# Optimization experiments

Measured on AMD Instinct MI355X. Metric: run time of the kernel, lower is better.

## Reference

```python
import jax, jax.numpy as jnp
import numpy as np

B, NX, NY, F = 4, 4096, 4096, 16

def setup_inputs() -> dict:
    key = jax.random.key(0)
    k1, k2, k3, k4, k5 = jax.random.split(key, 5)
    return {
        "x": jax.random.normal(k1, (B, NX, 3), dtype=jnp.float32),
        "y": jax.random.normal(k2, (B, NY, 3), dtype=jnp.float32),
        "sample_x": jax.random.uniform(k3, (B, NX, F), dtype=jnp.float32),
        "sample_y": jax.random.uniform(k4, (B, NY, F), dtype=jnp.float32),
        "scale": jax.random.uniform(k5, (F,), dtype=jnp.float32),
    }

def reference(x, y, sample_x, sample_y, scale):
    sq_x = jnp.sum(x * x, axis=-1, keepdims=True)            # (B,NX,1)
    sq_y = jnp.sum(y * y, axis=-1, keepdims=True)            # (B,NY,1)
    dot = jnp.einsum('bnd,bmd->bnm', x, y)                   # (B,NX,NY)
    d = jnp.clip(sq_x + jnp.swapaxes(sq_y, -2, -1) - 2.0 * dot, 1e-10, 1e6)
    # fixed-scale branch
    s = jnp.clip(scale, 1e-6, 1e6)
    scale_x = jnp.clip(jnp.einsum('bnf,f->bn', sample_x, s), 1e-10, 1e6)  # (B,NX)
    scale_y = jnp.clip(jnp.einsum('bmf,f->bm', sample_y, s), 1e-10, 1e6)  # (B,NY)
    scale_xy = jnp.sqrt(jnp.clip(scale_x[:, :, None] * scale_y[:, None, :], 1e-10, 1e12))
    return 1.0 / (1.0 + d / scale_xy)
```

## Files before the change

kernel.cpp:

```cpp
#include <hip/hip_runtime.h>


constexpr int kB  = 4;
constexpr int kNX = 4096;
constexpr int kNY = 4096;
constexpr int kF  = 16;

typedef float floatx4 __attribute__((ext_vector_type(4)));

__global__ __launch_bounds__(256) void row_stats_kernel(
    const float* __restrict__ x, const float* __restrict__ y,
    const float* __restrict__ sx, const float* __restrict__ sy,
    const float* __restrict__ scale,
    float2* __restrict__ rx, float2* __restrict__ ry, int nper)
{
    int t = blockIdx.x * blockDim.x + threadIdx.x;
    if (t >= 2 * nper) return;
    const float* pts; const float* smp; float2* dst; int idx;
    if (t < nper) { pts = x; smp = sx; dst = rx; idx = t; }
    else          { pts = y; smp = sy; dst = ry; idx = t - nper; }

    const float* p = pts + (size_t)idx * 3;
    float sq = p[0] * p[0] + p[1] * p[1] + p[2] * p[2];

    const float4* s4 = (const float4*)(smp + (size_t)idx * kF);
    const float4* c4 = (const float4*)scale;
    float acc = 0.f;
#pragma unroll
    for (int k = 0; k < kF / 4; ++k) {
        float4 sv = s4[k];
        float4 cv = c4[k];
        acc += sv.x * fminf(fmaxf(cv.x, 1e-6f), 1e6f);
        acc += sv.y * fminf(fmaxf(cv.y, 1e-6f), 1e6f);
        acc += sv.z * fminf(fmaxf(cv.z, 1e-6f), 1e6f);
        acc += sv.w * fminf(fmaxf(cv.w, 1e-6f), 1e6f);
    }
    float sc = fminf(fmaxf(acc, 1e-10f), 1e6f);
    dst[idx] = make_float2(sq, __builtin_amdgcn_sqrtf(sc));
}

__device__ __forceinline__ void cauchy_tile(
    int b, int i0, int j0,
    const float sqx[4], const float scx[4],
    const float sqy[4], const float scy[4],
    const float xxx[4], const float xyy[4], const float xzz[4],
    const float yxx[4], const float yyy[4], const float yzz[4],
    float* __restrict__ out)
{
    size_t obase = ((size_t)b * kNX + i0) * (size_t)kNY + j0;
#pragma unroll
    for (int r = 0; r < 4; ++r) {
        floatx4 o;
#pragma unroll
        for (int k = 0; k < 4; ++k) {
            float dot = xxx[r] * yxx[k] + xyy[r] * yyy[k] + xzz[r] * yzz[k];
            float d = fmaf(-2.f, dot, sqx[r] + sqy[k]);
            d = fminf(fmaxf(d, 1e-10f), 1e6f);
            float s = fmaxf(scx[r] * scy[k], 1e-5f);
            o[k] = s * __builtin_amdgcn_rcpf(s + d);
        }
        __builtin_nontemporal_store(o, (floatx4*)(out + obase + (size_t)r * kNY));
    }
}

__global__ __launch_bounds__(256) void cauchy_main_kernel(
    const float* __restrict__ x, const float* __restrict__ y,
    const float2* __restrict__ rx, const float2* __restrict__ ry,
    float* __restrict__ out)
{
    const int jc = ((blockIdx.x & 3) << 8) | threadIdx.x;
    const int rowtile = blockIdx.x >> 2;
    const int b  = rowtile >> 10;
    const int i0 = (rowtile & (kNX / 4 - 1)) << 2;
    const int j0 = jc << 2;

    const float4* yv = (const float4*)(y + ((size_t)b * kNY + j0) * 3);
    float4 ya = yv[0], yb = yv[1], yc = yv[2];
    const float4* ryv = (const float4*)(ry + (size_t)b * kNY + j0);
    float4 r01 = ryv[0], r23 = ryv[1];

    const float4* xv = (const float4*)(x + ((size_t)b * kNX + i0) * 3);
    float4 xa = xv[0], xb = xv[1], xc = xv[2];
    const float4* rxv = (const float4*)(rx + (size_t)b * kNX + i0);
    float4 q01 = rxv[0], q23 = rxv[1];

    const float yxx[4] = {ya.x, ya.w, yb.z, yc.y};
    const float yyy[4] = {ya.y, yb.x, yb.w, yc.z};
    const float yzz[4] = {ya.z, yb.y, yc.x, yc.w};
    const float sqy[4] = {r01.x, r01.z, r23.x, r23.z};
    const float scy[4] = {r01.y, r01.w, r23.y, r23.w};

    const float xxx[4] = {xa.x, xa.w, xb.z, xc.y};
    const float xyy[4] = {xa.y, xb.x, xb.w, xc.z};
    const float xzz[4] = {xa.z, xb.y, xc.x, xc.w};
    const float sqx[4] = {q01.x, q01.z, q23.x, q23.z};
    const float scx[4] = {q01.y, q01.w, q23.y, q23.w};

    cauchy_tile(b, i0, j0, sqx, scx, sqy, scy,
                xxx, xyy, xzz, yxx, yyy, yzz, out);
}

__global__ __launch_bounds__(256) void cauchy_fallback_kernel(
    const float* __restrict__ x, const float* __restrict__ y,
    const float* __restrict__ sx, const float* __restrict__ sy,
    const float* __restrict__ scale, float* __restrict__ out)
{
    const int jc = ((blockIdx.x & 3) << 8) | threadIdx.x;
    const int rowtile = blockIdx.x >> 2;
    const int b  = rowtile >> 10;
    const int i0 = (rowtile & (kNX / 4 - 1)) << 2;
    const int j0 = jc << 2;

    float4 c[4];
    const float4* c4 = (const float4*)scale;
#pragma unroll
    for (int k = 0; k < 4; ++k) {
        float4 cv = c4[k];
        c[k].x = fminf(fmaxf(cv.x, 1e-6f), 1e6f);
        c[k].y = fminf(fmaxf(cv.y, 1e-6f), 1e6f);
        c[k].z = fminf(fmaxf(cv.z, 1e-6f), 1e6f);
        c[k].w = fminf(fmaxf(cv.w, 1e-6f), 1e6f);
    }

    const float4* yv = (const float4*)(y + ((size_t)b * kNY + j0) * 3);
    float4 ya = yv[0], yb = yv[1], yc = yv[2];
    const float4* xv = (const float4*)(x + ((size_t)b * kNX + i0) * 3);
    float4 xa = xv[0], xb = xv[1], xc = xv[2];

    const float yxx[4] = {ya.x, ya.w, yb.z, yc.y};
    const float yyy[4] = {ya.y, yb.x, yb.w, yc.z};
    const float yzz[4] = {ya.z, yb.y, yc.x, yc.w};
    const float xxx[4] = {xa.x, xa.w, xb.z, xc.y};
    const float xyy[4] = {xa.y, xb.x, xb.w, xc.z};
    const float xzz[4] = {xa.z, xb.y, xc.x, xc.w};

    float sqx[4], scx[4], sqy[4], scy[4];
#pragma unroll
    for (int r = 0; r < 4; ++r) {
        sqx[r] = xxx[r] * xxx[r] + xyy[r] * xyy[r] + xzz[r] * xzz[r];
        sqy[r] = yxx[r] * yxx[r] + yyy[r] * yyy[r] + yzz[r] * yzz[r];
        const float4* a4 = (const float4*)(sx + ((size_t)b * kNX + i0 + r) * kF);
        const float4* b4 = (const float4*)(sy + ((size_t)b * kNY + j0 + r) * kF);
        float accx = 0.f, accy = 0.f;
#pragma unroll
        for (int k = 0; k < 4; ++k) {
            float4 av = a4[k], bv = b4[k], cv = c[k];
            accx += av.x * cv.x + av.y * cv.y + av.z * cv.z + av.w * cv.w;
            accy += bv.x * cv.x + bv.y * cv.y + bv.z * cv.z + bv.w * cv.w;
        }
        scx[r] = __builtin_amdgcn_sqrtf(fminf(fmaxf(accx, 1e-10f), 1e6f));
        scy[r] = __builtin_amdgcn_sqrtf(fminf(fmaxf(accy, 1e-10f), 1e6f));
    }

    cauchy_tile(b, i0, j0, sqx, scx, sqy, scy,
                xxx, xyy, xzz, yxx, yyy, yzz, out);
}

extern "C" void kernel_launch(void* const* d_in, const int* in_sizes, int n_in,
                              void* d_out, int out_size, void* d_ws, size_t ws_size,
                              hipStream_t stream) {
    const float* x     = (const float*)d_in[0];
    const float* y     = (const float*)d_in[1];
    const float* sx    = (const float*)d_in[2];
    const float* sy    = (const float*)d_in[3];
    const float* scale = (const float*)d_in[4];
    float* out = (float*)d_out;

    const int nper = kB * kNX;
    const size_t need = (size_t)2 * nper * sizeof(float2);
    const int main_blocks = (kB * kNX * kNY / 16) / 256;

    if (ws_size >= need) {
        float2* rx = (float2*)d_ws;
        float2* ry = rx + nper;
        row_stats_kernel<<<(2 * nper + 255) / 256, 256, 0, stream>>>(
            x, y, sx, sy, scale, rx, ry, nper);
        cauchy_main_kernel<<<main_blocks, 256, 0, stream>>>(x, y, rx, ry, out);
    } else {
        cauchy_fallback_kernel<<<main_blocks, 256, 0, stream>>>(
            x, y, sx, sy, scale, out);
    }
}
```

Measured before the change: 271.7 us.

## Fuse row stats into single kernel with XCD-aware block remap and plain stores

Removes the separate row-statistics pre-pass and workspace, so each thread recomputes squared norms and scale sums for its 4 x-rows and 4 y-columns from the raw sample arrays. Block indices are remapped so that consecutive logical tiles land on the same XCD, which is meant to improve L2 reuse of the x/y/sample inputs. The output stores change from nontemporal to ordinary vector stores. The cost is redundant per-thread dot products over 16 features and extra input reads, in exchange for dropping one launch and the round trip through workspace.

```diff
diff --git a/kernel.cpp b/kernel.cpp
--- a/kernel.cpp
+++ b/kernel.cpp
@@ -5,108 +5,19 @@
 constexpr int kNX = 4096;
 constexpr int kNY = 4096;
 constexpr int kF  = 16;
+constexpr int kNumXCD = 8;
 
-typedef float floatx4 __attribute__((ext_vector_type(4)));
-
-__global__ __launch_bounds__(256) void row_stats_kernel(
-    const float* __restrict__ x, const float* __restrict__ y,
-    const float* __restrict__ sx, const float* __restrict__ sy,
-    const float* __restrict__ scale,
-    float2* __restrict__ rx, float2* __restrict__ ry, int nper)
-{
-    int t = blockIdx.x * blockDim.x + threadIdx.x;
-    if (t >= 2 * nper) return;
-    const float* pts; const float* smp; float2* dst; int idx;
-    if (t < nper) { pts = x; smp = sx; dst = rx; idx = t; }
-    else          { pts = y; smp = sy; dst = ry; idx = t - nper; }
-
-    const float* p = pts + (size_t)idx * 3;
-    float sq = p[0] * p[0] + p[1] * p[1] + p[2] * p[2];
-
-    const float4* s4 = (const float4*)(smp + (size_t)idx * kF);
-    const float4* c4 = (const float4*)scale;
-    float acc = 0.f;
-#pragma unroll
-    for (int k = 0; k < kF / 4; ++k) {
-        float4 sv = s4[k];
-        float4 cv = c4[k];
-        acc += sv.x * fminf(fmaxf(cv.x, 1e-6f), 1e6f);
-        acc += sv.y * fminf(fmaxf(cv.y, 1e-6f), 1e6f);
-        acc += sv.z * fminf(fmaxf(cv.z, 1e-6f), 1e6f);
-        acc += sv.w * fminf(fmaxf(cv.w, 1e-6f), 1e6f);
-    }
-    float sc = fminf(fmaxf(acc, 1e-10f), 1e6f);
-    dst[idx] = make_float2(sq, __builtin_amdgcn_sqrtf(sc));
-}
-
-__device__ __forceinline__ void cauchy_tile(
-    int b, int i0, int j0,
-    const float sqx[4], const float scx[4],
-    const float sqy[4], const float scy[4],
-    const float xxx[4], const float xyy[4], const float xzz[4],
-    const float yxx[4], const float yyy[4], const float yzz[4],
-    float* __restrict__ out)
-{
-    size_t obase = ((size_t)b * kNX + i0) * (size_t)kNY + j0;
-#pragma unroll
-    for (int r = 0; r < 4; ++r) {
-        floatx4 o;
-#pragma unroll
-        for (int k = 0; k < 4; ++k) {
-            float dot = xxx[r] * yxx[k] + xyy[r] * yyy[k] + xzz[r] * yzz[k];
-            float d = fmaf(-2.f, dot, sqx[r] + sqy[k]);
-            d = fminf(fmaxf(d, 1e-10f), 1e6f);
-            float s = fmaxf(scx[r] * scy[k], 1e-5f);
-            o[k] = s * __builtin_amdgcn_rcpf(s + d);
-        }
-        __builtin_nontemporal_store(o, (floatx4*)(out + obase + (size_t)r * kNY));
-    }
-}
-
-__global__ __launch_bounds__(256) void cauchy_main_kernel(
-    const float* __restrict__ x, const float* __restrict__ y,
-    const float2* __restrict__ rx, const float2* __restrict__ ry,
-    float* __restrict__ out)
-{
-    const int jc = ((blockIdx.x & 3) << 8) | threadIdx.x;
-    const int rowtile = blockIdx.x >> 2;
-    const int b  = rowtile >> 10;
-    const int i0 = (rowtile & (kNX / 4 - 1)) << 2;
-    const int j0 = jc << 2;
-
-    const float4* yv = (const float4*)(y + ((size_t)b * kNY + j0) * 3);
-    float4 ya = yv[0], yb = yv[1], yc = yv[2];
-    const float4* ryv = (const float4*)(ry + (size_t)b * kNY + j0);
-    float4 r01 = ryv[0], r23 = ryv[1];
-
-    const float4* xv = (const float4*)(x + ((size_t)b * kNX + i0) * 3);
-    float4 xa = xv[0], xb = xv[1], xc = xv[2];
-    const float4* rxv = (const float4*)(rx + (size_t)b * kNX + i0);
-    float4 q01 = rxv[0], q23 = rxv[1];
-
-    const float yxx[4] = {ya.x, ya.w, yb.z, yc.y};
-    const float yyy[4] = {ya.y, yb.x, yb.w, yc.z};
-    const float yzz[4] = {ya.z, yb.y, yc.x, yc.w};
-    const float sqy[4] = {r01.x, r01.z, r23.x, r23.z};
-    const float scy[4] = {r01.y, r01.w, r23.y, r23.w};
-
-    const float xxx[4] = {xa.x, xa.w, xb.z, xc.y};
-    const float xyy[4] = {xa.y, xb.x, xb.w, xc.z};
-    const float xzz[4] = {xa.z, xb.y, xc.x, xc.w};
-    const float sqx[4] = {q01.x, q01.z, q23.x, q23.z};
-    const float scx[4] = {q01.y, q01.w, q23.y, q23.w};
-
-    cauchy_tile(b, i0, j0, sqx, scx, sqy, scy,
-                xxx, xyy, xzz, yxx, yyy, yzz, out);
-}
-
-__global__ __launch_bounds__(256) void cauchy_fallback_kernel(
+__global__ __launch_bounds__(256) void cauchy_fused_kernel(
     const float* __restrict__ x, const float* __restrict__ y,
     const float* __restrict__ sx, const float* __restrict__ sy,
     const float* __restrict__ scale, float* __restrict__ out)
 {
-    const int jc = ((blockIdx.x & 3) << 8) | threadIdx.x;
-    const int rowtile = blockIdx.x >> 2;
+    constexpr int kNBlk = (kB * kNX * kNY / 16) / 256;
+    const int hw = blockIdx.x;
+    const int logical = (hw % kNumXCD) * (kNBlk / kNumXCD) + hw / kNumXCD;
+
+    const int jc = ((logical & 3) << 8) | threadIdx.x;
+    const int rowtile = logical >> 2;
     const int b  = rowtile >> 10;
     const int i0 = (rowtile & (kNX / 4 - 1)) << 2;
     const int j0 = jc << 2;
@@ -145,15 +56,30 @@
 #pragma unroll
         for (int k = 0; k < 4; ++k) {
             float4 av = a4[k], bv = b4[k], cv = c[k];
-            accx += av.x * cv.x + av.y * cv.y + av.z * cv.z + av.w * cv.w;
-            accy += bv.x * cv.x + bv.y * cv.y + bv.z * cv.z + bv.w * cv.w;
+            accx += av.x * cv.x; accx += av.y * cv.y;
+            accx += av.z * cv.z; accx += av.w * cv.w;
+            accy += bv.x * cv.x; accy += bv.y * cv.y;
+            accy += bv.z * cv.z; accy += bv.w * cv.w;
         }
         scx[r] = __builtin_amdgcn_sqrtf(fminf(fmaxf(accx, 1e-10f), 1e6f));
         scy[r] = __builtin_amdgcn_sqrtf(fminf(fmaxf(accy, 1e-10f), 1e6f));
     }
 
-    cauchy_tile(b, i0, j0, sqx, scx, sqy, scy,
-                xxx, xyy, xzz, yxx, yyy, yzz, out);
+    size_t obase = ((size_t)b * kNX + i0) * (size_t)kNY + j0;
+#pragma unroll
+    for (int r = 0; r < 4; ++r) {
+        float4 o;
+        float* op = (float*)&o;
+#pragma unroll
+        for (int k = 0; k < 4; ++k) {
+            float dot = xxx[r] * yxx[k] + xyy[r] * yyy[k] + xzz[r] * yzz[k];
+            float d = fmaf(-2.f, dot, sqx[r] + sqy[k]);
+            d = fminf(fmaxf(d, 1e-10f), 1e6f);
+            float s = fmaxf(scx[r] * scy[k], 1e-5f);
+            op[k] = s * __builtin_amdgcn_rcpf(s + d);
+        }
+        *(float4*)(out + obase + (size_t)r * kNY) = o;
+    }
 }
 
 extern "C" void kernel_launch(void* const* d_in, const int* in_sizes, int n_in,
@@ -166,18 +92,7 @@
     const float* scale = (const float*)d_in[4];
     float* out = (float*)d_out;
 
-    const int nper = kB * kNX;
-    const size_t need = (size_t)2 * nper * sizeof(float2);
     const int main_blocks = (kB * kNX * kNY / 16) / 256;
-
-    if (ws_size >= need) {
-        float2* rx = (float2*)d_ws;
-        float2* ry = rx + nper;
-        row_stats_kernel<<<(2 * nper + 255) / 256, 256, 0, stream>>>(
-            x, y, sx, sy, scale, rx, ry, nper);
-        cauchy_main_kernel<<<main_blocks, 256, 0, stream>>>(x, y, rx, ry, out);
-    } else {
-        cauchy_fallback_kernel<<<main_blocks, 256, 0, stream>>>(
-            x, y, sx, sy, scale, out);
-    }
+    cauchy_fused_kernel<<<main_blocks, 256, 0, stream>>>(
+        x, y, sx, sy, scale, out);
 }
```

Measured after the change: 369.8 us. 1.36x slower.

## Use persistent-style grid looping over batches and row halves, drop nontemporal stores

Applied to the files above, without the earlier changes.

The main kernel launches a fixed 2048 blocks instead of one block per 4-row tile. Each thread loops over all batches and two row halves, reusing its loaded y data and stats across the rows it handles. Output stores change from nontemporal to plain float4 stores. The aim is to cut block scheduling overhead and redundant y loads, at the cost of fewer resident waves and more serial work per thread on a store-bound kernel.

```diff
diff --git a/kernel.cpp b/kernel.cpp
--- a/kernel.cpp
+++ b/kernel.cpp
@@ -5,8 +5,6 @@
 constexpr int kNX = 4096;
 constexpr int kNY = 4096;
 constexpr int kF  = 16;
-
-typedef float floatx4 __attribute__((ext_vector_type(4)));
 
 __global__ __launch_bounds__(256) void row_stats_kernel(
     const float* __restrict__ x, const float* __restrict__ y,
@@ -39,65 +37,61 @@
     dst[idx] = make_float2(sq, __builtin_amdgcn_sqrtf(sc));
 }
 
-__device__ __forceinline__ void cauchy_tile(
-    int b, int i0, int j0,
-    const float sqx[4], const float scx[4],
-    const float sqy[4], const float scy[4],
-    const float xxx[4], const float xyy[4], const float xzz[4],
-    const float yxx[4], const float yyy[4], const float yzz[4],
-    float* __restrict__ out)
-{
-    size_t obase = ((size_t)b * kNX + i0) * (size_t)kNY + j0;
-#pragma unroll
-    for (int r = 0; r < 4; ++r) {
-        floatx4 o;
-#pragma unroll
-        for (int k = 0; k < 4; ++k) {
-            float dot = xxx[r] * yxx[k] + xyy[r] * yyy[k] + xzz[r] * yzz[k];
-            float d = fmaf(-2.f, dot, sqx[r] + sqy[k]);
-            d = fminf(fmaxf(d, 1e-10f), 1e6f);
-            float s = fmaxf(scx[r] * scy[k], 1e-5f);
-            o[k] = s * __builtin_amdgcn_rcpf(s + d);
-        }
-        __builtin_nontemporal_store(o, (floatx4*)(out + obase + (size_t)r * kNY));
-    }
-}
-
 __global__ __launch_bounds__(256) void cauchy_main_kernel(
     const float* __restrict__ x, const float* __restrict__ y,
     const float2* __restrict__ rx, const float2* __restrict__ ry,
     float* __restrict__ out)
 {
-    const int jc = ((blockIdx.x & 3) << 8) | threadIdx.x;
-    const int rowtile = blockIdx.x >> 2;
-    const int b  = rowtile >> 10;
-    const int i0 = (rowtile & (kNX / 4 - 1)) << 2;
-    const int j0 = jc << 2;
+    const int hw   = blockIdx.x;
+    const int jc   = ((hw & 3) << 8) | threadIdx.x;
+    const int j0   = jc << 2;
+    const int qrow = hw >> 2;
 
-    const float4* yv = (const float4*)(y + ((size_t)b * kNY + j0) * 3);
-    float4 ya = yv[0], yb = yv[1], yc = yv[2];
-    const float4* ryv = (const float4*)(ry + (size_t)b * kNY + j0);
-    float4 r01 = ryv[0], r23 = ryv[1];
+#pragma unroll 1
+    for (int bb = 0; bb < kB; ++bb) {
+        const float4* yv = (const float4*)(y + ((size_t)bb * kNY + j0) * 3);
+        float4 ya = yv[0], yb = yv[1], yc = yv[2];
+        const float4* ryv = (const float4*)(ry + (size_t)bb * kNY + j0);
+        float4 r01 = ryv[0], r23 = ryv[1];
 
-    const float4* xv = (const float4*)(x + ((size_t)b * kNX + i0) * 3);
-    float4 xa = xv[0], xb = xv[1], xc = xv[2];
-    const float4* rxv = (const float4*)(rx + (size_t)b * kNX + i0);
-    float4 q01 = rxv[0], q23 = rxv[1];
+        const float yxx[4] = {ya.x, ya.w, yb.z, yc.y};
+        const float yyy[4] = {ya.y, yb.x, yb.w, yc.z};
+        const float yzz[4] = {ya.z, yb.y, yc.x, yc.w};
+        const float sqy[4] = {r01.x, r01.z, r23.x, r23.z};
+        const float scy[4] = {r01.y, r01.w, r23.y, r23.w};
 
-    const float yxx[4] = {ya.x, ya.w, yb.z, yc.y};
-    const float yyy[4] = {ya.y, yb.x, yb.w, yc.z};
-    const float yzz[4] = {ya.z, yb.y, yc.x, yc.w};
-    const float sqy[4] = {r01.x, r01.z, r23.x, r23.z};
-    const float scy[4] = {r01.y, r01.w, r23.y, r23.w};
+#pragma unroll
+        for (int h = 0; h < 2; ++h) {
+            const int i0 = ((h << 9) | qrow) << 2;
 
-    const float xxx[4] = {xa.x, xa.w, xb.z, xc.y};
-    const float xyy[4] = {xa.y, xb.x, xb.w, xc.z};
-    const float xzz[4] = {xa.z, xb.y, xc.x, xc.w};
-    const float sqx[4] = {q01.x, q01.z, q23.x, q23.z};
-    const float scx[4] = {q01.y, q01.w, q23.y, q23.w};
+            const float4* xv = (const float4*)(x + ((size_t)bb * kNX + i0) * 3);
+            float4 xa = xv[0], xb = xv[1], xc = xv[2];
+            const float4* rxv = (const float4*)(rx + (size_t)bb * kNX + i0);
+            float4 q01 = rxv[0], q23 = rxv[1];
 
-    cauchy_tile(b, i0, j0, sqx, scx, sqy, scy,
-                xxx, xyy, xzz, yxx, yyy, yzz, out);
+            const float xxx[4] = {xa.x, xa.w, xb.z, xc.y};
+            const float xyy[4] = {xa.y, xb.x, xb.w, xc.z};
+            const float xzz[4] = {xa.z, xb.y, xc.x, xc.w};
+            const float sqx[4] = {q01.x, q01.z, q23.x, q23.z};
+            const float scx[4] = {q01.y, q01.w, q23.y, q23.w};
+
+            size_t obase = ((size_t)bb * kNX + i0) * (size_t)kNY + j0;
+#pragma unroll
+            for (int r = 0; r < 4; ++r) {
+                float4 o;
+                float* op = (float*)&o;
+#pragma unroll
+                for (int k = 0; k < 4; ++k) {
+                    float dot = xxx[r] * yxx[k] + xyy[r] * yyy[k] + xzz[r] * yzz[k];
+                    float d = fmaf(-2.f, dot, sqx[r] + sqy[k]);
+                    d = fminf(fmaxf(d, 1e-10f), 1e6f);
+                    float s = fmaxf(scx[r] * scy[k], 1e-5f);
+                    op[k] = s * __builtin_amdgcn_rcpf(s + d);
+                }
+                *(float4*)(out + obase + (size_t)r * kNY) = o;
+            }
+        }
+    }
 }
 
 __global__ __launch_bounds__(256) void cauchy_fallback_kernel(
@@ -105,8 +99,9 @@
     const float* __restrict__ sx, const float* __restrict__ sy,
     const float* __restrict__ scale, float* __restrict__ out)
 {
-    const int jc = ((blockIdx.x & 3) << 8) | threadIdx.x;
-    const int rowtile = blockIdx.x >> 2;
+    const int t = blockIdx.x * 256 + threadIdx.x;
+    const int jc = t & (kNY / 4 - 1);
+    const int rowtile = t >> 10;
     const int b  = rowtile >> 10;
     const int i0 = (rowtile & (kNX / 4 - 1)) << 2;
     const int j0 = jc << 2;
@@ -152,8 +147,21 @@
         scy[r] = __builtin_amdgcn_sqrtf(fminf(fmaxf(accy, 1e-10f), 1e6f));
     }
 
-    cauchy_tile(b, i0, j0, sqx, scx, sqy, scy,
-                xxx, xyy, xzz, yxx, yyy, yzz, out);
+    size_t obase = ((size_t)b * kNX + i0) * (size_t)kNY + j0;
+#pragma unroll
+    for (int r = 0; r < 4; ++r) {
+        float4 o;
+        float* op = (float*)&o;
+#pragma unroll
+        for (int k = 0; k < 4; ++k) {
+            float dot = xxx[r] * yxx[k] + xyy[r] * yyy[k] + xzz[r] * yzz[k];
+            float d = fmaf(-2.f, dot, sqx[r] + sqy[k]);
+            d = fminf(fmaxf(d, 1e-10f), 1e6f);
+            float s = fmaxf(scx[r] * scy[k], 1e-5f);
+            op[k] = s * __builtin_amdgcn_rcpf(s + d);
+        }
+        *(float4*)(out + obase + (size_t)r * kNY) = o;
+    }
 }
 
 extern "C" void kernel_launch(void* const* d_in, const int* in_sizes, int n_in,
@@ -168,16 +176,16 @@
 
     const int nper = kB * kNX;
     const size_t need = (size_t)2 * nper * sizeof(float2);
-    const int main_blocks = (kB * kNX * kNY / 16) / 256;
 
     if (ws_size >= need) {
         float2* rx = (float2*)d_ws;
         float2* ry = rx + nper;
         row_stats_kernel<<<(2 * nper + 255) / 256, 256, 0, stream>>>(
             x, y, sx, sy, scale, rx, ry, nper);
-        cauchy_main_kernel<<<main_blocks, 256, 0, stream>>>(x, y, rx, ry, out);
+        cauchy_main_kernel<<<2048, 256, 0, stream>>>(x, y, rx, ry, out);
     } else {
-        cauchy_fallback_kernel<<<main_blocks, 256, 0, stream>>>(
+        const int fb_blocks = (kB * kNX * kNY / 16) / 256;
+        cauchy_fallback_kernel<<<fb_blocks, 256, 0, stream>>>(
             x, y, sx, sy, scale, out);
     }
 }
```

Measured after the change: 263.0 us. 3.2% less time.
